# Optimization experiments

Hardware: AMD Instinct MI355X
Metric: run time of the kernel (lower is better)

## Reference

```python
import jax, jax.numpy as jnp
from jax import lax
import numpy as np

SEQ, BATCH, HID = 1024, 2048, 64

def setup_inputs() -> dict:
    key = jax.random.key(0)
    ks = jax.random.split(key, 9)
    s = 1.0 / np.sqrt(HID)
    return {
        "x": jax.random.normal(ks[0], (SEQ, BATCH), dtype=jnp.float32),
        "W_ih": jax.random.uniform(ks[1], (4 * HID, 1), jnp.float32, -s, s),
        "W_hh": jax.random.uniform(ks[2], (4 * HID, HID), jnp.float32, -s, s),
        "b_ih": jax.random.uniform(ks[3], (4 * HID,), jnp.float32, -s, s),
        "b_hh": jax.random.uniform(ks[4], (4 * HID,), jnp.float32, -s, s),
        "fc1_w": jax.random.uniform(ks[5], (128, HID), jnp.float32, -s, s),
        "fc1_b": jax.random.uniform(ks[6], (128,), jnp.float32, -s, s),
        "fc2_w": jax.random.uniform(ks[7], (5, 128), jnp.float32, -s, s),
        "fc2_b": jax.random.uniform(ks[8], (5,), jnp.float32, -s, s),
    }

def reference(x, W_ih, W_hh, b_ih, b_hh, fc1_w, fc1_b, fc2_w, fc2_b):
    # x: (S, B) -> unsqueeze(2) gives (S, B, 1); input_size == 1 so the input
    # projection is an outer product, precomputed for all timesteps at once.
    # gx: (S, B, 4H), gate order i, f, g, o (PyTorch convention)
    gx = x[:, :, None] * W_ih[:, 0][None, None, :] + b_ih

    B = x.shape[1]
    h0 = jnp.zeros((B, HID), dtype=x.dtype)
    c0 = jnp.zeros((B, HID), dtype=x.dtype)

    def step(carry, g):
        h, c = carry
        gates = g + h @ W_hh.T + b_hh  # (B, 4H)
        i, f, gg, o = jnp.split(gates, 4, axis=-1)
        i = jax.nn.sigmoid(i)
        f = jax.nn.sigmoid(f)
        gg = jnp.tanh(gg)
        o = jax.nn.sigmoid(o)
        c = f * c + i * gg
        h = o * jnp.tanh(c)
        return (h, c), None

    (h_n, c_n), _ = lax.scan(step, (h0, c0), gx)
    # Original uses hidden[1] == cell state c_n for the MLP head (no activation).
    out = (c_n @ fc1_w.T + fc1_b) @ fc2_w.T + fc2_b  # (B, 5)
    return out
```

## Files before the change

### kernel.cpp

```cpp
#include <hip/hip_runtime.h>
#include <hip/hip_bf16.h>

#define S_LEN 1024
#define BATCH 2048
#define HID   64
#define MB    4
#define NBLK  (BATCH / MB)
#define NTHR  (MB * HID)

typedef _Float16 half8 __attribute__((ext_vector_type(8)));
typedef float    f32x4 __attribute__((ext_vector_type(4)));

#define L2E 1.4426950408889634f
#define HSTRIDE 72

__global__ __launch_bounds__(NTHR) void lstm_kernel(
    const float* __restrict__ x,
    const float* __restrict__ W_ih,
    const float* __restrict__ W_hh,
    const float* __restrict__ b_ih,
    const float* __restrict__ b_hh,
    const float* __restrict__ fc1_w,
    const float* __restrict__ fc1_b,
    const float* __restrict__ fc2_w,
    const float* __restrict__ fc2_b,
    float* __restrict__ out)
{
    __shared__ __align__(16) _Float16 h_buf[2][4 * HSTRIDE];
    __shared__ __align__(16) float    head_lds[MB * HID + MB * 128];

    const int tid  = threadIdx.x;
    const int lane = tid & 63;
    const int wave = tid >> 6;
    const int l15  = lane & 15;
    const int quad = lane >> 4;
    const int b0   = blockIdx.x * MB;

    {
        unsigned* hz = (unsigned*)&h_buf[0][0];
        for (int i = tid; i < 2 * 4 * HSTRIDE / 2; i += NTHR) hz[i] = 0u;
    }

    half8 wfrag[4][2];
    #pragma unroll
    for (int g = 0; g < 4; ++g) {
        const float s = (g == 2) ? (-2.0f * L2E) : (-L2E);
        const float* wr = W_hh + (g * 64 + 16 * wave + l15) * HID + quad * 8;
        #pragma unroll
        for (int kt = 0; kt < 2; ++kt) {
            half8 f;
            #pragma unroll
            for (int j = 0; j < 8; ++j) f[j] = (_Float16)(wr[kt * 32 + j] * s);
            wfrag[g][kt] = f;
        }
    }

    const int u = 16 * wave + l15;
    float wih_s[4], bias_s[4];
    #pragma unroll
    for (int g = 0; g < 4; ++g) {
        const int n = g * 64 + u;
        const float s = (g == 2) ? (-2.0f * L2E) : (-L2E);
        wih_s[g]  = W_ih[n] * s;
        bias_s[g] = (b_ih[n] + b_hh[n]) * s;
    }

    const float* xcol = x + b0 + quad;
    float c = 0.0f;

    float xq[4];
    #pragma unroll
    for (int j = 0; j < 4; ++j) xq[j] = xcol[(size_t)j * BATCH];

    __syncthreads();

    auto body = [&](int base, int j, const _Float16* hr, _Float16* hw) {
        const float xv = xq[j];
        int sp = base + j + 4;
        if (sp > S_LEN - 1) sp = S_LEN - 1;
        xq[j] = xcol[(size_t)sp * BATCH];

        const _Float16* arow = hr + (l15 >> 2) * HSTRIDE + quad * 8;
        half8 a0 = *(const half8*)(arow);
        half8 a1 = *(const half8*)(arow + 32);

        f32x4 acc[4];
        #pragma unroll
        for (int g = 0; g < 4; ++g) {
            f32x4 a = {0.f, 0.f, 0.f, 0.f};
            a = __builtin_amdgcn_mfma_f32_16x16x32_f16(a0, wfrag[g][0], a, 0, 0, 0);
            a = __builtin_amdgcn_mfma_f32_16x16x32_f16(a1, wfrag[g][1], a, 0, 0, 0);
            acc[g] = a;
        }

        const float gi = acc[0][0] + __builtin_fmaf(xv, wih_s[0], bias_s[0]);
        const float gf = acc[1][0] + __builtin_fmaf(xv, wih_s[1], bias_s[1]);
        const float gg = acc[2][0] + __builtin_fmaf(xv, wih_s[2], bias_s[2]);
        const float go = acc[3][0] + __builtin_fmaf(xv, wih_s[3], bias_s[3]);

        const float i_ = __builtin_amdgcn_rcpf(1.0f + __builtin_amdgcn_exp2f(gi));
        const float f_ = __builtin_amdgcn_rcpf(1.0f + __builtin_amdgcn_exp2f(gf));
        const float g_ = 2.0f * __builtin_amdgcn_rcpf(1.0f + __builtin_amdgcn_exp2f(gg)) - 1.0f;
        const float o_ = __builtin_amdgcn_rcpf(1.0f + __builtin_amdgcn_exp2f(go));

        c = f_ * c + i_ * g_;
        const float th = 2.0f * __builtin_amdgcn_rcpf(
                             1.0f + __builtin_amdgcn_exp2f((-2.0f * L2E) * c)) - 1.0f;
        const float h = o_ * th;

        hw[quad * HSTRIDE + u] = (_Float16)h;
        __syncthreads();
    };

    _Float16* h0 = &h_buf[0][0];
    _Float16* h1 = &h_buf[1][0];

    for (int base = 0; base < S_LEN; base += 4) {
        body(base, 0, h0, h1);
        body(base, 1, h1, h0);
        body(base, 2, h0, h1);
        body(base, 3, h1, h0);
    }

    float* c_lds  = head_lds;
    float* h1_lds = head_lds + MB * HID;
    c_lds[quad * HID + u] = c;
    __syncthreads();

    for (int idx = tid; idx < MB * 128; idx += NTHR) {
        const int b = idx >> 7, j = idx & 127;
        const float* wrow = fc1_w + j * HID;
        const float* crow = c_lds + b * HID;
        float acc = fc1_b[j];
        #pragma unroll
        for (int k = 0; k < HID; k += 4)
            acc += crow[k] * wrow[k] + crow[k+1] * wrow[k+1]
                 + crow[k+2] * wrow[k+2] + crow[k+3] * wrow[k+3];
        h1_lds[idx] = acc;
    }
    __syncthreads();

    if (tid < MB * 5) {
        const int b = tid / 5, q = tid % 5;
        const float* wrow = fc2_w + q * 128;
        const float* hrow = h1_lds + b * 128;
        float acc = fc2_b[q];
        #pragma unroll 4
        for (int j = 0; j < 128; ++j) acc += hrow[j] * wrow[j];
        out[(b0 + b) * 5 + q] = acc;
    }
}

extern "C" void kernel_launch(void* const* d_in, const int* in_sizes, int n_in,
                              void* d_out, int out_size, void* d_ws, size_t ws_size,
                              hipStream_t stream) {
    const float* x     = (const float*)d_in[0];
    const float* W_ih  = (const float*)d_in[1];
    const float* W_hh  = (const float*)d_in[2];
    const float* b_ih  = (const float*)d_in[3];
    const float* b_hh  = (const float*)d_in[4];
    const float* fc1_w = (const float*)d_in[5];
    const float* fc1_b = (const float*)d_in[6];
    const float* fc2_w = (const float*)d_in[7];
    const float* fc2_b = (const float*)d_in[8];
    float* out = (float*)d_out;

    lstm_kernel<<<NBLK, NTHR, 0, stream>>>(x, W_ih, W_hh, b_ih, b_hh,
                                           fc1_w, fc1_b, fc2_w, fc2_b, out);
}
```

Before: 341.5 us.

## Preload block's x column slice into LDS and precompute h-buffer pointers

Each block now loads its entire 1024x4 x slice into shared memory up front with float4 loads, replacing the per-step global prefetch with an LDS read inside the recurrence. LDS read and write addresses for the double-buffered h are precomputed, and the loop unroll drops from 4 to 2. Launch bounds now request 2 blocks per SIMD. This aims to take global-memory latency off the serial critical path, at the cost of 16KB extra LDS per block and a startup load phase.

```diff
diff --git a/kernel.cpp b/kernel.cpp
--- a/kernel.cpp
+++ b/kernel.cpp
@@ -10,11 +10,12 @@
 
 typedef _Float16 half8 __attribute__((ext_vector_type(8)));
 typedef float    f32x4 __attribute__((ext_vector_type(4)));
+typedef float    f32x4a __attribute__((ext_vector_type(4))) __attribute__((aligned(16)));
 
 #define L2E 1.4426950408889634f
 #define HSTRIDE 72
 
-__global__ __launch_bounds__(NTHR) void lstm_kernel(
+__global__ __launch_bounds__(NTHR, 2) void lstm_kernel(
     const float* __restrict__ x,
     const float* __restrict__ W_ih,
     const float* __restrict__ W_hh,
@@ -26,7 +27,8 @@
     const float* __restrict__ fc2_b,
     float* __restrict__ out)
 {
-    __shared__ __align__(16) _Float16 h_buf[2][4 * HSTRIDE];
+    __shared__ __align__(16) float    xs[S_LEN * MB];
+    __shared__ __align__(16) _Float16 h_buf[2][MB * HSTRIDE];
     __shared__ __align__(16) float    head_lds[MB * HID + MB * 128];
 
     const int tid  = threadIdx.x;
@@ -37,8 +39,17 @@
     const int b0   = blockIdx.x * MB;
 
     {
+        float4* xs4 = (float4*)xs;
+        #pragma unroll
+        for (int t = 0; t < 4; ++t) {
+            const int s = tid + 256 * t;
+            xs4[s] = *(const float4*)(x + (size_t)s * BATCH + b0);
+        }
+    }
+
+    {
         unsigned* hz = (unsigned*)&h_buf[0][0];
-        for (int i = tid; i < 2 * 4 * HSTRIDE / 2; i += NTHR) hz[i] = 0u;
+        for (int i = tid; i < 2 * MB * HSTRIDE / 2; i += NTHR) hz[i] = 0u;
     }
 
     half8 wfrag[4][2];
@@ -65,32 +76,28 @@
         bias_s[g] = (b_ih[n] + b_hh[n]) * s;
     }
 
-    const float* xcol = x + b0 + quad;
     float c = 0.0f;
+    const f32x4 zero4 = {0.f, 0.f, 0.f, 0.f};
 
-    float xq[4];
-    #pragma unroll
-    for (int j = 0; j < 4; ++j) xq[j] = xcol[(size_t)j * BATCH];
+    const _Float16* a0p = &h_buf[0][0] + (l15 >> 2) * HSTRIDE + quad * 8;
+    const _Float16* a1p = &h_buf[1][0] + (l15 >> 2) * HSTRIDE + quad * 8;
+    _Float16* w0p = &h_buf[0][0] + quad * HSTRIDE + u;
+    _Float16* w1p = &h_buf[1][0] + quad * HSTRIDE + u;
+    const float* xp = xs + quad;
 
     __syncthreads();
 
-    auto body = [&](int base, int j, const _Float16* hr, _Float16* hw) {
-        const float xv = xq[j];
-        int sp = base + j + 4;
-        if (sp > S_LEN - 1) sp = S_LEN - 1;
-        xq[j] = xcol[(size_t)sp * BATCH];
+    auto body = [&](int s, const _Float16* ar, _Float16* hw) {
+        const float xv = xp[4 * s];
 
-        const _Float16* arow = hr + (l15 >> 2) * HSTRIDE + quad * 8;
-        half8 a0 = *(const half8*)(arow);
-        half8 a1 = *(const half8*)(arow + 32);
+        half8 a0 = *(const half8*)(ar);
+        half8 a1 = *(const half8*)(ar + 32);
 
         f32x4 acc[4];
         #pragma unroll
         for (int g = 0; g < 4; ++g) {
-            f32x4 a = {0.f, 0.f, 0.f, 0.f};
-            a = __builtin_amdgcn_mfma_f32_16x16x32_f16(a0, wfrag[g][0], a, 0, 0, 0);
-            a = __builtin_amdgcn_mfma_f32_16x16x32_f16(a1, wfrag[g][1], a, 0, 0, 0);
-            acc[g] = a;
+            acc[g] = __builtin_amdgcn_mfma_f32_16x16x32_f16(a0, wfrag[g][0], zero4, 0, 0, 0);
+            acc[g] = __builtin_amdgcn_mfma_f32_16x16x32_f16(a1, wfrag[g][1], acc[g], 0, 0, 0);
         }
 
         const float gi = acc[0][0] + __builtin_fmaf(xv, wih_s[0], bias_s[0]);
@@ -108,18 +115,13 @@
                              1.0f + __builtin_amdgcn_exp2f((-2.0f * L2E) * c)) - 1.0f;
         const float h = o_ * th;
 
-        hw[quad * HSTRIDE + u] = (_Float16)h;
+        hw[0] = (_Float16)h;
         __syncthreads();
     };
 
-    _Float16* h0 = &h_buf[0][0];
-    _Float16* h1 = &h_buf[1][0];
-
-    for (int base = 0; base < S_LEN; base += 4) {
-        body(base, 0, h0, h1);
-        body(base, 1, h1, h0);
-        body(base, 2, h0, h1);
-        body(base, 3, h1, h0);
+    for (int s = 0; s < S_LEN; s += 2) {
+        body(s,     a0p, w1p);
+        body(s + 1, a1p, w0p);
     }
 
     float* c_lds  = head_lds;
```

New measurement: 335.0 us. Within noise of the previous version (-1.9%).
